# Optimization experiments

Measured on AMD Instinct MI355X. Metric: run time of the kernel, lower is better.

The kernel has to match this reference:

```python
import jax, jax.numpy as jnp
import numpy as np

N_NODES = 100000
N_EDGES = 1600000
D_IN = 256
D_HID = 128
N_CLASSES = 64
NEG_SLOPE = 0.2


def setup_inputs() -> dict:
    key = jax.random.key(0)
    ks = jax.random.split(key, 8)
    node_features = jax.random.normal(ks[0], (N_NODES, D_IN), dtype=jnp.float32)
    W = jax.random.normal(ks[1], (D_IN, D_HID), dtype=jnp.float32) * (1.0 / np.sqrt(D_IN))
    attn_l = jax.random.normal(ks[2], (D_HID,), dtype=jnp.float32) * (1.0 / np.sqrt(D_HID))
    attn_r = jax.random.normal(ks[3], (D_HID,), dtype=jnp.float32) * (1.0 / np.sqrt(D_HID))
    fc_W = jax.random.normal(ks[4], (D_HID, N_CLASSES), dtype=jnp.float32) * (1.0 / np.sqrt(D_HID))
    fc_b = jnp.zeros((N_CLASSES,), dtype=jnp.float32)
    src = jax.random.randint(ks[5], (N_EDGES,), 0, N_NODES, dtype=jnp.int32)
    dst = jax.random.randint(ks[6], (N_EDGES,), 0, N_NODES, dtype=jnp.int32)
    return dict(node_features=node_features, W=W, attn_l=attn_l, attn_r=attn_r,
                fc_W=fc_W, fc_b=fc_b, src=src, dst=dst)


def reference(node_features, W, attn_l, attn_r, fc_W, fc_b, src, dst):
    N = node_features.shape[0]
    # GATConv (single head): linear projection
    feat = node_features @ W                       # [N, H]
    el = feat @ attn_l                             # [N]
    er = feat @ attn_r                             # [N]
    e = jax.nn.leaky_relu(el[src] + er[dst], NEG_SLOPE)  # [E]
    # segment softmax over incoming edges of each destination node
    m = jax.ops.segment_max(e, dst, num_segments=N)      # [N]
    ex = jnp.exp(e - m[dst])                              # [E]
    denom = jax.ops.segment_sum(ex, dst, num_segments=N)  # [N]
    a = ex / denom[dst]                                   # [E]
    # attention-weighted neighbor aggregation (scatter-add)
    msg = a[:, None] * feat[src]                           # [E, H]
    h = jax.ops.segment_sum(msg, dst, num_segments=N)     # [N, H]
    # num_heads=1 -> h.mean(1) over heads is identity; final Linear
    return h @ fc_W + fc_b                                 # [N, C]
```

## Files before the change

### kernel.cpp

```cpp
#include <hip/hip_runtime.h>
#include <math.h>

#define NN 100000
#define NE 1600000
#define DIN 256
#define DHID 128
#define NCLS 64
#define NEG_SLOPE 0.2f

#define NBUCK 196
#define ECAP 10240
#define CHUNK 4096
#define NCHB ((NE + CHUNK - 1) / CHUNK)
#define PREPB 16

#define NGRP 16384
#define G1 ((NN + 127) / 128)

typedef __bf16 bf16_t;
typedef bf16_t bf16x8 __attribute__((ext_vector_type(8)));
typedef float f32x4 __attribute__((ext_vector_type(4)));
typedef ushort ushort8v __attribute__((ext_vector_type(8)));

__device__ __forceinline__ ushort f2bf(float f) {
    union { float f; unsigned u; } c; c.f = f;
    unsigned u = c.u;
    unsigned r = (u + 0x7FFFu + ((u >> 16) & 1u)) >> 16;
    return (ushort)r;
}
__device__ __forceinline__ float bf2f(ushort b) {
    return __uint_as_float(((unsigned)b) << 16);
}

__global__ __launch_bounds__(256) void k_prep(const float* __restrict__ W,
                                              const float* __restrict__ fcW,
                                              ushort* __restrict__ Wt,
                                              ushort* __restrict__ fcWt,
                                              int* __restrict__ gcur) {
    int t = blockIdx.x * 256 + threadIdx.x;
    if (blockIdx.x == 0) gcur[threadIdx.x] = 0;
    for (int i = t; i < DHID * DIN; i += PREPB * 256) {
        int n = i >> 8, k = i & 255;
        Wt[i] = f2bf(W[k * DHID + n]);
    }
    for (int i = t; i < NCLS * DHID; i += PREPB * 256) {
        int n = i >> 7, k = i & 127;
        fcWt[i] = f2bf(fcW[k * NCLS + n]);
    }
}

union SmemB {
    struct {
        int hist[NBUCK];
        int scn[256];
        int loff[NBUCK];
        int cur[NBUCK];
        int gb[NBUCK];
        unsigned ord[CHUNK];
        ushort obk[CHUNK];
    } b;
    struct {
        ushort Xs[2][8192];
        ushort Wl[2][8192];
        float Al[DHID];
        float Ar[DHID];
    } g;
};

__global__ __launch_bounds__(256, 2) void fused_bin_gemm1(
        const int* __restrict__ src, const int* __restrict__ dst,
        int* __restrict__ gcur, unsigned* __restrict__ ebuf,
        const float* __restrict__ X, const ushort* __restrict__ Wt,
        const float* __restrict__ attn_l, const float* __restrict__ attn_r,
        ushort* __restrict__ featb, float* __restrict__ el, float* __restrict__ er) {
    __shared__ SmemB sm;
    const int t = threadIdx.x;

    if (blockIdx.x < NCHB) {
        const int base = blockIdx.x * CHUNK;
        int cnt = NE - base; if (cnt > CHUNK) cnt = CHUNK;

        for (int i = t; i < NBUCK; i += 256) sm.b.hist[i] = 0;
        __syncthreads();

        unsigned vals[16];
        int bks[16];
#pragma unroll
        for (int i = 0; i < 16; i++) {
            int idx = base + i * 256 + t;
            if (idx < NE) {
                int d = dst[idx], s = src[idx];
                int bb = d >> 9;
                bks[i] = bb;
                vals[i] = ((unsigned)(d & 511) << 17) | (unsigned)s;
                atomicAdd(&sm.b.hist[bb], 1);
            } else bks[i] = -1;
        }
        __syncthreads();

        int hv = (t < NBUCK) ? sm.b.hist[t] : 0;
        sm.b.scn[t] = hv;
        __syncthreads();
        for (int d = 1; d < 256; d <<= 1) {
            int a = (t >= d) ? sm.b.scn[t - d] : 0;
            __syncthreads();
            sm.b.scn[t] += a;
            __syncthreads();
        }
        if (t < NBUCK) { sm.b.loff[t] = sm.b.scn[t] - hv; sm.b.cur[t] = sm.b.scn[t] - hv; }
        __syncthreads();

#pragma unroll
        for (int i = 0; i < 16; i++) {
            if (bks[i] >= 0) {
                int slot = atomicAdd(&sm.b.cur[bks[i]], 1);
                sm.b.ord[slot] = vals[i];
                sm.b.obk[slot] = (ushort)bks[i];
            }
        }
        if (t < NBUCK && hv > 0) sm.b.gb[t] = t * ECAP + atomicAdd(&gcur[t], hv);
        __syncthreads();

        for (int s = t; s < cnt; s += 256) {
            int bb = sm.b.obk[s];
            ebuf[sm.b.gb[bb] + (s - sm.b.loff[bb])] = sm.b.ord[s];
        }
        return;
    }

    const int row0 = (blockIdx.x - NCHB) * 128;
    if (t < 128) { sm.g.Al[t] = attn_l[t]; sm.g.Ar[t] = attn_r[t]; }

    int srow[4], ske[4];
#pragma unroll
    for (int i = 0; i < 4; i++) {
        int o = i * 4096 + t * 16;
        int row = o >> 7;
        int bl = (o & 127) ^ ((row & 7) << 4);
        srow[i] = row;
        ske[i] = bl >> 1;
    }

    float4 xr[4][2];
    uint4  wr[4];

#pragma unroll
    for (int i = 0; i < 4; i++) {
        int grow = row0 + srow[i];
        if (grow < NN) {
            const float4* p = (const float4*)(X + (size_t)grow * DIN + ske[i]);
            xr[i][0] = p[0]; xr[i][1] = p[1];
        } else {
            xr[i][0] = make_float4(0.f, 0.f, 0.f, 0.f);
            xr[i][1] = make_float4(0.f, 0.f, 0.f, 0.f);
        }
        wr[i] = *(const uint4*)(Wt + (size_t)srow[i] * DIN + ske[i]);
    }
#pragma unroll
    for (int i = 0; i < 4; i++) {
        int o = i * 4096 + t * 16;
        ushort8v b;
        b[0] = f2bf(xr[i][0].x); b[1] = f2bf(xr[i][0].y);
        b[2] = f2bf(xr[i][0].z); b[3] = f2bf(xr[i][0].w);
        b[4] = f2bf(xr[i][1].x); b[5] = f2bf(xr[i][1].y);
        b[6] = f2bf(xr[i][1].z); b[7] = f2bf(xr[i][1].w);
        *(ushort8v*)((char*)&sm.g.Xs[0][0] + o) = b;
        *(uint4*)((char*)&sm.g.Wl[0][0] + o) = wr[i];
    }
    __syncthreads();

    const int w = t >> 6, lane = t & 63;
    const int rbase = w * 32;
    const int lcol = lane & 15;
    const int kgrp = (lane >> 4) * 16;

    f32x4 acc[2][8];
#pragma unroll
    for (int r = 0; r < 2; r++)
#pragma unroll
        for (int c = 0; c < 8; c++) acc[r][c] = (f32x4){0.f, 0.f, 0.f, 0.f};

    for (int c = 0; c < 4; c++) {
        const int buf = c & 1;
        if (c < 3) {
            int k0g = (c + 1) * 64;
#pragma unroll
            for (int i = 0; i < 4; i++) {
                int grow = row0 + srow[i];
                if (grow < NN) {
                    const float4* p = (const float4*)(X + (size_t)grow * DIN + k0g + ske[i]);
                    xr[i][0] = p[0]; xr[i][1] = p[1];
                } else {
                    xr[i][0] = make_float4(0.f, 0.f, 0.f, 0.f);
                    xr[i][1] = make_float4(0.f, 0.f, 0.f, 0.f);
                }
                wr[i] = *(const uint4*)(Wt + (size_t)srow[i] * DIN + k0g + ske[i]);
            }
        }
        const char* xb = (const char*)&sm.g.Xs[buf][0];
        const char* wb = (const char*)&sm.g.Wl[buf][0];
#pragma unroll
        for (int k0 = 0; k0 < 2; k0++) {
            int kb = k0 * 64 + kgrp;
            bf16x8 a[2], b[8];
#pragma unroll
            for (int r = 0; r < 2; r++) {
                int row = rbase + r * 16 + lcol;
                a[r] = *(const bf16x8*)(xb + row * 128 + (kb ^ ((row & 7) << 4)));
            }
#pragma unroll
            for (int cc = 0; cc < 8; cc++) {
                int n = cc * 16 + lcol;
                b[cc] = *(const bf16x8*)(wb + n * 128 + (kb ^ ((n & 7) << 4)));
            }
#pragma unroll
            for (int r = 0; r < 2; r++)
#pragma unroll
                for (int cc = 0; cc < 8; cc++)
                    acc[r][cc] = __builtin_amdgcn_mfma_f32_16x16x32_bf16(a[r], b[cc], acc[r][cc], 0, 0, 0);
        }
        if (c < 3) {
#pragma unroll
            for (int i = 0; i < 4; i++) {
                int o = i * 4096 + t * 16;
                ushort8v b;
                b[0] = f2bf(xr[i][0].x); b[1] = f2bf(xr[i][0].y);
                b[2] = f2bf(xr[i][0].z); b[3] = f2bf(xr[i][0].w);
                b[4] = f2bf(xr[i][1].x); b[5] = f2bf(xr[i][1].y);
                b[6] = f2bf(xr[i][1].z); b[7] = f2bf(xr[i][1].w);
                *(ushort8v*)((char*)&sm.g.Xs[buf ^ 1][0] + o) = b;
                *(uint4*)((char*)&sm.g.Wl[buf ^ 1][0] + o) = wr[i];
            }
        }
        __syncthreads();
    }

    ushort* Os = (ushort*)sm.g.Xs;
#pragma unroll
    for (int r = 0; r < 2; r++)
#pragma unroll
        for (int cc = 0; cc < 8; cc++)
#pragma unroll
            for (int i = 0; i < 4; i++) {
                int rloc = rbase + r * 16 + (lane >> 4) * 4 + i;
                int col = cc * 16 + lcol;
                Os[rloc * 128 + col] = f2bf(acc[r][cc][i]);
            }
    __syncthreads();

    {
        int row = t >> 1, half = t & 1;
        int grow = row0 + row;
        const ushort* orow = Os + row * 128 + half * 64;
        const float* alp = sm.g.Al + half * 64;
        const float* arp = sm.g.Ar + half * 64;
        float pl = 0.f, pr = 0.f;
        int rot = row & 7;
#pragma unroll
        for (int qq = 0; qq < 8; qq++) {
            int q = (qq + rot) & 7;
            ushort8v f8 = *(const ushort8v*)(orow + q * 8);
#pragma unroll
            for (int e = 0; e < 8; e++) {
                float fe = bf2f(f8[e]);
                pl += fe * alp[q * 8 + e];
                pr += fe * arp[q * 8 + e];
            }
        }
        pl += __shfl_down(pl, 1);
        pr += __shfl_down(pr, 1);
        if (!half && grow < NN) { el[grow] = pl; er[grow] = pr; }
    }

#pragma unroll
    for (int i = 0; i < 8; i++) {
        int u = i * 256 + t;
        int row = u >> 4;
        int grow = row0 + row;
        if (grow < NN)
            *(uint4*)(featb + (size_t)grow * 128 + (u & 15) * 8) =
                *(uint4*)((char*)Os + u * 16);
    }
}

union SmemC {
    struct {
        int sdeg[512];
        int pr[256];
        int lofs[512];
        int scnt[512];
    } c;
    int sh[256];
};

__global__ __launch_bounds__(256) void fused_csr(const unsigned* __restrict__ ebuf,
                                                 const int* __restrict__ gcur,
                                                 int* __restrict__ off_g,
                                                 int* __restrict__ deg_g,
                                                 int* __restrict__ ssrc,
                                                 int* __restrict__ bpre) {
    __shared__ SmemC sm;
    const int t = threadIdx.x;

    if (blockIdx.x == NBUCK) {
        int v = (t < NBUCK) ? gcur[t] : 0;
        sm.sh[t] = v;
        __syncthreads();
        for (int d = 1; d < 256; d <<= 1) {
            int a = (t >= d) ? sm.sh[t - d] : 0;
            __syncthreads();
            sm.sh[t] += a;
            __syncthreads();
        }
        if (t < NBUCK) bpre[t] = sm.sh[t] - v;
        if (t == NBUCK - 1) bpre[NBUCK] = sm.sh[t];
        return;
    }

    const int b = blockIdx.x;
    const int node0 = b << 9;
    const int ebase = b * ECAP;
    const int ecnt = gcur[b];

    sm.c.sdeg[t] = 0; sm.c.sdeg[t + 256] = 0;
    __syncthreads();
    for (int s = t; s < ecnt; s += 256)
        atomicAdd(&sm.c.sdeg[ebuf[ebase + s] >> 17], 1);
    __syncthreads();

    int d0 = sm.c.sdeg[2 * t], d1 = sm.c.sdeg[2 * t + 1];
    sm.c.pr[t] = d0 + d1;
    __syncthreads();
    for (int d = 1; d < 256; d <<= 1) {
        int a = (t >= d) ? sm.c.pr[t - d] : 0;
        __syncthreads();
        sm.c.pr[t] += a;
        __syncthreads();
    }
    int ex = sm.c.pr[t] - d0 - d1;
    sm.c.lofs[2 * t] = ex;
    sm.c.lofs[2 * t + 1] = ex + d0;
    sm.c.scnt[2 * t] = 0; sm.c.scnt[2 * t + 1] = 0;
    int n0 = node0 + 2 * t, n1 = n0 + 1;
    if (n0 < NN) { off_g[n0] = ebase + ex;      deg_g[n0] = d0; }
    if (n1 < NN) { off_g[n1] = ebase + ex + d0; deg_g[n1] = d1; }
    __syncthreads();

    for (int s = t; s < ecnt; s += 256) {
        unsigned v = ebuf[ebase + s];
        int dl = v >> 17;
        int c = atomicAdd(&sm.c.scnt[dl], 1);
        ssrc[ebase + sm.c.lofs[dl] + c] = (int)(v & 0x1FFFFu);
    }
}

__device__ __forceinline__ int find_node(const int* __restrict__ off,
                                         const int* __restrict__ bpre,
                                         long target) {
    int lo = 0, hi = NN;
    while (lo < hi) {
        int mid = (lo + hi) >> 1;
        int b = mid >> 9;
        long real = (long)off[mid] - (long)b * ECAP + bpre[b];
        if (real < target) lo = mid + 1; else hi = mid;
    }
    return lo;
}

__global__ __launch_bounds__(256) void aggregate(const int* __restrict__ off,
                                                 const int* __restrict__ deg,
                                                 const int* __restrict__ ssrc,
                                                 const float* __restrict__ el,
                                                 const float* __restrict__ er,
                                                 const ushort* __restrict__ featb,
                                                 ushort* __restrict__ hb,
                                                 const int* __restrict__ bpre) {
    const int gid = blockIdx.x * 16 + (threadIdx.x >> 4);
    const int lc = threadIdx.x & 15;
    const long total = bpre[NBUCK];
    int n = find_node(off, bpre, (long)gid * total / NGRP);
    const int nend = find_node(off, bpre, (long)(gid + 1) * total / NGRP);
    const ushort* fb = featb + lc * 8;

    for (; n < nend; ++n) {
        const int e0 = off[n];
        const int dg = deg[n];
        const float erd = er[n];
        float acc[8];
#pragma unroll
        for (int q = 0; q < 8; q++) acc[q] = 0.f;
        float wsum = 0.f;

        int j = 0;
        for (; j + 4 <= dg; j += 4) {
            int s0 = ssrc[e0 + j + 0];
            int s1 = ssrc[e0 + j + 1];
            int s2 = ssrc[e0 + j + 2];
            int s3 = ssrc[e0 + j + 3];
            ushort8v f0 = *(const ushort8v*)(fb + (size_t)s0 * DHID);
            ushort8v f1 = *(const ushort8v*)(fb + (size_t)s1 * DHID);
            ushort8v f2 = *(const ushort8v*)(fb + (size_t)s2 * DHID);
            ushort8v f3 = *(const ushort8v*)(fb + (size_t)s3 * DHID);
            float x0 = el[s0] + erd, x1 = el[s1] + erd;
            float x2 = el[s2] + erd, x3 = el[s3] + erd;
            x0 = x0 > 0.f ? x0 : NEG_SLOPE * x0;
            x1 = x1 > 0.f ? x1 : NEG_SLOPE * x1;
            x2 = x2 > 0.f ? x2 : NEG_SLOPE * x2;
            x3 = x3 > 0.f ? x3 : NEG_SLOPE * x3;
            float w0 = __expf(x0), w1 = __expf(x1);
            float w2 = __expf(x2), w3 = __expf(x3);
            wsum += (w0 + w1) + (w2 + w3);
#pragma unroll
            for (int q = 0; q < 8; q++)
                acc[q] += (w0 * bf2f(f0[q]) + w1 * bf2f(f1[q])) +
                          (w2 * bf2f(f2[q]) + w3 * bf2f(f3[q]));
        }
        for (; j < dg; ++j) {
            int s0 = ssrc[e0 + j];
            ushort8v f0 = *(const ushort8v*)(fb + (size_t)s0 * DHID);
            float x0 = el[s0] + erd;
            x0 = x0 > 0.f ? x0 : NEG_SLOPE * x0;
            float w0 = __expf(x0);
            wsum += w0;
#pragma unroll
            for (int q = 0; q < 8; q++) acc[q] += w0 * bf2f(f0[q]);
        }

        float inv = (dg > 0) ? 1.0f / wsum : 0.f;
        ushort8v o8;
#pragma unroll
        for (int q = 0; q < 8; q++) o8[q] = f2bf(acc[q] * inv);
        *(ushort8v*)(hb + (size_t)n * DHID + lc * 8) = o8;
    }
}

__global__ __launch_bounds__(256) void gemm2(const ushort* __restrict__ hb,
                                             const ushort* __restrict__ fcWt,
                                             const float* __restrict__ fcb,
                                             float* __restrict__ out) {
    __shared__ ushort Hs[128 * 128];
    __shared__ ushort Fs[64 * 128];
    const int t = threadIdx.x;
    const int row0 = blockIdx.x * 128;

    {
#pragma unroll
        for (int i = 0; i < 8; i++) {
            int u = i * 256 + t;
            int row = u >> 4;
            int grow = row0 + row;
            uint4 v = make_uint4(0, 0, 0, 0);
            if (grow < NN) v = *(const uint4*)(hb + (size_t)grow * 128 + (u & 15) * 8);
            int byte_off = row * 256 + (((u & 15) * 16) ^ ((row & 7) << 4));
            *(uint4*)((char*)Hs + byte_off) = v;
        }
#pragma unroll
        for (int i = 0; i < 4; i++) {
            int u = i * 256 + t;
            int n = u >> 4;
            int byte_off = n * 256 + (((u & 15) * 16) ^ ((n & 7) << 4));
            *(uint4*)((char*)Fs + byte_off) = ((const uint4*)fcWt)[u];
        }
    }

    const int w = t >> 6, lane = t & 63;
    const int rbase = w * 32;
    const int lcol = lane & 15;
    const int kgrp = (lane >> 4) * 16;

    f32x4 acc[2][4];
#pragma unroll
    for (int c = 0; c < 4; c++) {
        float bias = fcb[c * 16 + lcol];
#pragma unroll
        for (int r = 0; r < 2; r++)
#pragma unroll
            for (int i = 0; i < 4; i++) acc[r][c][i] = bias;
    }
    __syncthreads();

#pragma unroll
    for (int k0 = 0; k0 < 4; k0++) {
        int kbyte = k0 * 64 + kgrp;
        bf16x8 a[2], b[4];
#pragma unroll
        for (int r = 0; r < 2; r++) {
            int row = rbase + r * 16 + lcol;
            a[r] = *(bf16x8*)((char*)Hs + row * 256 + (kbyte ^ ((row & 7) << 4)));
        }
#pragma unroll
        for (int c = 0; c < 4; c++) {
            int n = c * 16 + lcol;
            b[c] = *(bf16x8*)((char*)Fs + n * 256 + (kbyte ^ ((n & 7) << 4)));
        }
#pragma unroll
        for (int r = 0; r < 2; r++)
#pragma unroll
            for (int c = 0; c < 4; c++)
                acc[r][c] = __builtin_amdgcn_mfma_f32_16x16x32_bf16(a[r], b[c], acc[r][c], 0, 0, 0);
    }

#pragma unroll
    for (int r = 0; r < 2; r++)
#pragma unroll
        for (int i = 0; i < 4; i++) {
            int row = rbase + r * 16 + (lane >> 4) * 4 + i;
            int grow = row0 + row;
            if (grow < NN) {
                float* op = out + (size_t)grow * 64 + lcol;
#pragma unroll
                for (int c = 0; c < 4; c++) op[c * 16] = acc[r][c][i];
            }
        }
}

extern "C" void kernel_launch(void* const* d_in, const int* in_sizes, int n_in,
                              void* d_out, int out_size, void* d_ws, size_t ws_size,
                              hipStream_t stream) {
    const float* X      = (const float*)d_in[0];
    const float* W      = (const float*)d_in[1];
    const float* attn_l = (const float*)d_in[2];
    const float* attn_r = (const float*)d_in[3];
    const float* fcW    = (const float*)d_in[4];
    const float* fcb    = (const float*)d_in[5];
    const int*   src    = (const int*)d_in[6];
    const int*   dst    = (const int*)d_in[7];
    float* out = (float*)d_out;

    char* ws = (char*)d_ws;
    ushort* featb = (ushort*)ws;            ws += (size_t)NN * DHID * 2;
    ushort* hb    = (ushort*)ws;            ws += (size_t)NN * DHID * 2;
    ushort* Wt    = (ushort*)ws;            ws += (size_t)DHID * DIN * 2;
    ushort* fcWt  = (ushort*)ws;            ws += (size_t)NCLS * DHID * 2;
    float* el     = (float*)ws;             ws += (size_t)NN * 4;
    float* er     = (float*)ws;             ws += (size_t)NN * 4;
    int*   deg    = (int*)ws;               ws += (size_t)NN * 4;
    int*   off    = (int*)ws;               ws += (size_t)NN * 4;
    int*   ssrc   = (int*)ws;               ws += (size_t)NBUCK * ECAP * 4;
    unsigned* ebuf = (unsigned*)ws;         ws += (size_t)NBUCK * ECAP * 4;
    int*   gcur   = (int*)ws;               ws += (size_t)256 * 4;
    int*   bpre   = (int*)ws;               ws += (size_t)256 * 4;

    k_prep<<<PREPB, 256, 0, stream>>>(W, fcW, Wt, fcWt, gcur);
    fused_bin_gemm1<<<NCHB + G1, 256, 0, stream>>>(src, dst, gcur, ebuf,
                                                   X, Wt, attn_l, attn_r, featb, el, er);
    fused_csr<<<NBUCK + 1, 256, 0, stream>>>(ebuf, gcur, off, deg, ssrc, bpre);
    aggregate<<<NGRP / 16, 256, 0, stream>>>(off, deg, ssrc, el, er, featb, hb, bpre);
    gemm2<<<(NN + 127) / 128, 256, 0, stream>>>(hb, fcWt, fcb, out);
}
```

Measured before the change: 160.4 us.

## Regroup kernels: fuse binning with weight prep, GEMM1 with CSR build

The weight transpose/convert kernel is folded into the edge-binning kernel as extra blocks, and the CSR construction moves into the GEMM1 launch. GEMM1 now loads X and W fragments straight from global memory into registers with a software pipeline, dropping the LDS staging buffers and per-stage barriers. gcur is zeroed with a memset, and gemm2 gets an occupancy hint in its launch bounds. The aim is fewer launches and better overlap of independent work, at the cost of uncoalesced direct-to-register loads and more register pressure in GEMM1.

Measured after the change: 170.4 us. +6.2%, slower.

```diff
diff --git a/kernel.cpp b/kernel.cpp
--- a/kernel.cpp
+++ b/kernel.cpp
@@ -31,25 +31,14 @@
 __device__ __forceinline__ float bf2f(ushort b) {
     return __uint_as_float(((unsigned)b) << 16);
 }
-
-__global__ __launch_bounds__(256) void k_prep(const float* __restrict__ W,
-                                              const float* __restrict__ fcW,
-                                              ushort* __restrict__ Wt,
-                                              ushort* __restrict__ fcWt,
-                                              int* __restrict__ gcur) {
-    int t = blockIdx.x * 256 + threadIdx.x;
-    if (blockIdx.x == 0) gcur[threadIdx.x] = 0;
-    for (int i = t; i < DHID * DIN; i += PREPB * 256) {
-        int n = i >> 8, k = i & 255;
-        Wt[i] = f2bf(W[k * DHID + n]);
-    }
-    for (int i = t; i < NCLS * DHID; i += PREPB * 256) {
-        int n = i >> 7, k = i & 127;
-        fcWt[i] = f2bf(fcW[k * NCLS + n]);
-    }
-}
-
-union SmemB {
+__device__ __forceinline__ bf16x8 cvt8(float4 a, float4 b) {
+    union { ushort8v u; bf16x8 h; } c;
+    c.u[0] = f2bf(a.x); c.u[1] = f2bf(a.y); c.u[2] = f2bf(a.z); c.u[3] = f2bf(a.w);
+    c.u[4] = f2bf(b.x); c.u[5] = f2bf(b.y); c.u[6] = f2bf(b.z); c.u[7] = f2bf(b.w);
+    return c.h;
+}
+
+union SmemA {
     struct {
         int hist[NBUCK];
         int scn[256];
@@ -59,191 +48,221 @@
         unsigned ord[CHUNK];
         ushort obk[CHUNK];
     } b;
+};
+
+__global__ __launch_bounds__(256) void fused_bin_prep(
+        const int* __restrict__ src, const int* __restrict__ dst,
+        int* __restrict__ gcur, unsigned* __restrict__ ebuf,
+        const float* __restrict__ W, const float* __restrict__ fcW,
+        ushort* __restrict__ Wt, ushort* __restrict__ fcWt) {
+    __shared__ SmemA sm;
+    const int t = threadIdx.x;
+
+    if (blockIdx.x >= NCHB) {
+        int t0 = (blockIdx.x - NCHB) * 256 + t;
+        for (int i = t0; i < DHID * DIN; i += PREPB * 256) {
+            int n = i >> 8, k = i & 255;
+            Wt[i] = f2bf(W[k * DHID + n]);
+        }
+        for (int i = t0; i < NCLS * DHID; i += PREPB * 256) {
+            int n = i >> 7, k = i & 127;
+            fcWt[i] = f2bf(fcW[k * NCLS + n]);
+        }
+        return;
+    }
+
+    const int base = blockIdx.x * CHUNK;
+    int cnt = NE - base; if (cnt > CHUNK) cnt = CHUNK;
+
+    for (int i = t; i < NBUCK; i += 256) sm.b.hist[i] = 0;
+    __syncthreads();
+
+    unsigned vals[16];
+    int bks[16];
+#pragma unroll
+    for (int i = 0; i < 16; i++) {
+        int idx = base + i * 256 + t;
+        if (idx < NE) {
+            int d = dst[idx], s = src[idx];
+            int bb = d >> 9;
+            bks[i] = bb;
+            vals[i] = ((unsigned)(d & 511) << 17) | (unsigned)s;
+            atomicAdd(&sm.b.hist[bb], 1);
+        } else bks[i] = -1;
+    }
+    __syncthreads();
+
+    int hv = (t < NBUCK) ? sm.b.hist[t] : 0;
+    sm.b.scn[t] = hv;
+    __syncthreads();
+    for (int d = 1; d < 256; d <<= 1) {
+        int a = (t >= d) ? sm.b.scn[t - d] : 0;
+        __syncthreads();
+        sm.b.scn[t] += a;
+        __syncthreads();
+    }
+    if (t < NBUCK) { sm.b.loff[t] = sm.b.scn[t] - hv; sm.b.cur[t] = sm.b.scn[t] - hv; }
+    __syncthreads();
+
+#pragma unroll
+    for (int i = 0; i < 16; i++) {
+        if (bks[i] >= 0) {
+            int slot = atomicAdd(&sm.b.cur[bks[i]], 1);
+            sm.b.ord[slot] = vals[i];
+            sm.b.obk[slot] = (ushort)bks[i];
+        }
+    }
+    if (t < NBUCK && hv > 0) sm.b.gb[t] = t * ECAP + atomicAdd(&gcur[t], hv);
+    __syncthreads();
+
+    for (int s = t; s < cnt; s += 256) {
+        int bb = sm.b.obk[s];
+        ebuf[sm.b.gb[bb] + (s - sm.b.loff[bb])] = sm.b.ord[s];
+    }
+}
+
+union SmemB {
     struct {
-        ushort Xs[2][8192];
-        ushort Wl[2][8192];
+        ushort Os[128 * 128];
         float Al[DHID];
         float Ar[DHID];
     } g;
+    struct {
+        int sdeg[512];
+        int pr[256];
+        int lofs[512];
+        int scnt[512];
+    } c;
+    int sh[256];
 };
 
-__global__ __launch_bounds__(256, 2) void fused_bin_gemm1(
-        const int* __restrict__ src, const int* __restrict__ dst,
-        int* __restrict__ gcur, unsigned* __restrict__ ebuf,
+#define LOADX(B, KS) do { \
+    if (v0) { xa[B][0][0] = *(const float4*)(xb0 + (KS) * 32); \
+              xa[B][0][1] = *(const float4*)(xb0 + (KS) * 32 + 4); } \
+    else { xa[B][0][0] = make_float4(0.f,0.f,0.f,0.f); xa[B][0][1] = make_float4(0.f,0.f,0.f,0.f); } \
+    if (v1) { xa[B][1][0] = *(const float4*)(xb1 + (KS) * 32); \
+              xa[B][1][1] = *(const float4*)(xb1 + (KS) * 32 + 4); } \
+    else { xa[B][1][0] = make_float4(0.f,0.f,0.f,0.f); xa[B][1][1] = make_float4(0.f,0.f,0.f,0.f); } \
+} while (0)
+
+#define LOADW(B, KS) do { \
+    _Pragma("unroll") \
+    for (int cc = 0; cc < 8; cc++) \
+        bw[B][cc] = *(const bf16x8*)(wb + cc * 4096 + (KS) * 32); \
+} while (0)
+
+#define GITER(KS) do { \
+    if ((KS) + 1 < 8) LOADW(((KS) + 1) & 1, (KS) + 1); \
+    { bf16x8 af0 = cvt8(xa[(KS) % 3][0][0], xa[(KS) % 3][0][1]); \
+      bf16x8 af1 = cvt8(xa[(KS) % 3][1][0], xa[(KS) % 3][1][1]); \
+      _Pragma("unroll") \
+      for (int cc = 0; cc < 8; cc++) { \
+          acc[0][cc] = __builtin_amdgcn_mfma_f32_16x16x32_bf16(af0, bw[(KS) & 1][cc], acc[0][cc], 0, 0, 0); \
+          acc[1][cc] = __builtin_amdgcn_mfma_f32_16x16x32_bf16(af1, bw[(KS) & 1][cc], acc[1][cc], 0, 0, 0); } } \
+    if ((KS) + 3 < 8) LOADX((KS) % 3, (KS) + 3); \
+} while (0)
+
+__global__ __launch_bounds__(256, 2) void fused_g1_csr(
         const float* __restrict__ X, const ushort* __restrict__ Wt,
         const float* __restrict__ attn_l, const float* __restrict__ attn_r,
-        ushort* __restrict__ featb, float* __restrict__ el, float* __restrict__ er) {
+        ushort* __restrict__ featb, float* __restrict__ el, float* __restrict__ er,
+        const unsigned* __restrict__ ebuf, const int* __restrict__ gcur,
+        int* __restrict__ off_g, int* __restrict__ deg_g,
+        int* __restrict__ ssrc, int* __restrict__ bpre) {
     __shared__ SmemB sm;
     const int t = threadIdx.x;
 
-    if (blockIdx.x < NCHB) {
-        const int base = blockIdx.x * CHUNK;
-        int cnt = NE - base; if (cnt > CHUNK) cnt = CHUNK;
-
-        for (int i = t; i < NBUCK; i += 256) sm.b.hist[i] = 0;
-        __syncthreads();
-
-        unsigned vals[16];
-        int bks[16];
-#pragma unroll
-        for (int i = 0; i < 16; i++) {
-            int idx = base + i * 256 + t;
-            if (idx < NE) {
-                int d = dst[idx], s = src[idx];
-                int bb = d >> 9;
-                bks[i] = bb;
-                vals[i] = ((unsigned)(d & 511) << 17) | (unsigned)s;
-                atomicAdd(&sm.b.hist[bb], 1);
-            } else bks[i] = -1;
-        }
-        __syncthreads();
-
-        int hv = (t < NBUCK) ? sm.b.hist[t] : 0;
-        sm.b.scn[t] = hv;
+    if (blockIdx.x >= G1 + NBUCK) {
+        int v = (t < NBUCK) ? gcur[t] : 0;
+        sm.sh[t] = v;
         __syncthreads();
         for (int d = 1; d < 256; d <<= 1) {
-            int a = (t >= d) ? sm.b.scn[t - d] : 0;
+            int a = (t >= d) ? sm.sh[t - d] : 0;
             __syncthreads();
-            sm.b.scn[t] += a;
+            sm.sh[t] += a;
             __syncthreads();
         }
-        if (t < NBUCK) { sm.b.loff[t] = sm.b.scn[t] - hv; sm.b.cur[t] = sm.b.scn[t] - hv; }
-        __syncthreads();
-
-#pragma unroll
-        for (int i = 0; i < 16; i++) {
-            if (bks[i] >= 0) {
-                int slot = atomicAdd(&sm.b.cur[bks[i]], 1);
-                sm.b.ord[slot] = vals[i];
-                sm.b.obk[slot] = (ushort)bks[i];
-            }
-        }
-        if (t < NBUCK && hv > 0) sm.b.gb[t] = t * ECAP + atomicAdd(&gcur[t], hv);
-        __syncthreads();
-
-        for (int s = t; s < cnt; s += 256) {
-            int bb = sm.b.obk[s];
-            ebuf[sm.b.gb[bb] + (s - sm.b.loff[bb])] = sm.b.ord[s];
-        }
+        if (t < NBUCK) bpre[t] = sm.sh[t] - v;
+        if (t == NBUCK - 1) bpre[NBUCK] = sm.sh[t];
         return;
     }
 
-    const int row0 = (blockIdx.x - NCHB) * 128;
+    if (blockIdx.x >= G1) {
+        const int b = blockIdx.x - G1;
+        const int node0 = b << 9;
+        const int ebase = b * ECAP;
+        const int ecnt = gcur[b];
+
+        sm.c.sdeg[t] = 0; sm.c.sdeg[t + 256] = 0;
+        __syncthreads();
+        for (int s = t; s < ecnt; s += 256)
+            atomicAdd(&sm.c.sdeg[ebuf[ebase + s] >> 17], 1);
+        __syncthreads();
+
+        int d0 = sm.c.sdeg[2 * t], d1 = sm.c.sdeg[2 * t + 1];
+        sm.c.pr[t] = d0 + d1;
+        __syncthreads();
+        for (int d = 1; d < 256; d <<= 1) {
+            int a = (t >= d) ? sm.c.pr[t - d] : 0;
+            __syncthreads();
+            sm.c.pr[t] += a;
+            __syncthreads();
+        }
+        int ex = sm.c.pr[t] - d0 - d1;
+        sm.c.lofs[2 * t] = ex;
+        sm.c.lofs[2 * t + 1] = ex + d0;
+        sm.c.scnt[2 * t] = 0; sm.c.scnt[2 * t + 1] = 0;
+        int n0 = node0 + 2 * t, n1 = n0 + 1;
+        if (n0 < NN) { off_g[n0] = ebase + ex;      deg_g[n0] = d0; }
+        if (n1 < NN) { off_g[n1] = ebase + ex + d0; deg_g[n1] = d1; }
+        __syncthreads();
+
+        for (int s = t; s < ecnt; s += 256) {
+            unsigned v = ebuf[ebase + s];
+            int dl = v >> 17;
+            int c = atomicAdd(&sm.c.scnt[dl], 1);
+            ssrc[ebase + sm.c.lofs[dl] + c] = (int)(v & 0x1FFFFu);
+        }
+        return;
+    }
+
+    const int row0 = blockIdx.x * 128;
     if (t < 128) { sm.g.Al[t] = attn_l[t]; sm.g.Ar[t] = attn_r[t]; }
-
-    int srow[4], ske[4];
-#pragma unroll
-    for (int i = 0; i < 4; i++) {
-        int o = i * 4096 + t * 16;
-        int row = o >> 7;
-        int bl = (o & 127) ^ ((row & 7) << 4);
-        srow[i] = row;
-        ske[i] = bl >> 1;
-    }
-
-    float4 xr[4][2];
-    uint4  wr[4];
-
-#pragma unroll
-    for (int i = 0; i < 4; i++) {
-        int grow = row0 + srow[i];
-        if (grow < NN) {
-            const float4* p = (const float4*)(X + (size_t)grow * DIN + ske[i]);
-            xr[i][0] = p[0]; xr[i][1] = p[1];
-        } else {
-            xr[i][0] = make_float4(0.f, 0.f, 0.f, 0.f);
-            xr[i][1] = make_float4(0.f, 0.f, 0.f, 0.f);
-        }
-        wr[i] = *(const uint4*)(Wt + (size_t)srow[i] * DIN + ske[i]);
-    }
-#pragma unroll
-    for (int i = 0; i < 4; i++) {
-        int o = i * 4096 + t * 16;
-        ushort8v b;
-        b[0] = f2bf(xr[i][0].x); b[1] = f2bf(xr[i][0].y);
-        b[2] = f2bf(xr[i][0].z); b[3] = f2bf(xr[i][0].w);
-        b[4] = f2bf(xr[i][1].x); b[5] = f2bf(xr[i][1].y);
-        b[6] = f2bf(xr[i][1].z); b[7] = f2bf(xr[i][1].w);
-        *(ushort8v*)((char*)&sm.g.Xs[0][0] + o) = b;
-        *(uint4*)((char*)&sm.g.Wl[0][0] + o) = wr[i];
-    }
-    __syncthreads();
 
     const int w = t >> 6, lane = t & 63;
     const int rbase = w * 32;
-    const int lcol = lane & 15;
-    const int kgrp = (lane >> 4) * 16;
-
+    const int lc16 = lane & 15;
+    const int kg = lane >> 4;
+
+    const int arow0 = row0 + rbase + lc16;
+    const int arow1 = arow0 + 16;
+    const bool v0 = arow0 < NN, v1 = arow1 < NN;
+    const float* xb0 = X + (size_t)arow0 * DIN + kg * 8;
+    const float* xb1 = X + (size_t)arow1 * DIN + kg * 8;
+    const ushort* wb = Wt + (size_t)lc16 * DIN + kg * 8;
+
+    float4 xa[3][2][2];
+    bf16x8 bw[2][8];
     f32x4 acc[2][8];
 #pragma unroll
     for (int r = 0; r < 2; r++)
 #pragma unroll
         for (int c = 0; c < 8; c++) acc[r][c] = (f32x4){0.f, 0.f, 0.f, 0.f};
 
-    for (int c = 0; c < 4; c++) {
-        const int buf = c & 1;
-        if (c < 3) {
-            int k0g = (c + 1) * 64;
+    LOADX(0, 0); LOADX(1, 1); LOADX(2, 2);
+    LOADW(0, 0);
+    GITER(0); GITER(1); GITER(2); GITER(3);
+    GITER(4); GITER(5); GITER(6); GITER(7);
+
+    ushort* Os = sm.g.Os;
+#pragma unroll
+    for (int r = 0; r < 2; r++)
+#pragma unroll
+        for (int cc = 0; cc < 8; cc++)
 #pragma unroll
             for (int i = 0; i < 4; i++) {
-                int grow = row0 + srow[i];
-                if (grow < NN) {
-                    const float4* p = (const float4*)(X + (size_t)grow * DIN + k0g + ske[i]);
-                    xr[i][0] = p[0]; xr[i][1] = p[1];
-                } else {
-                    xr[i][0] = make_float4(0.f, 0.f, 0.f, 0.f);
-                    xr[i][1] = make_float4(0.f, 0.f, 0.f, 0.f);
-                }
-                wr[i] = *(const uint4*)(Wt + (size_t)srow[i] * DIN + k0g + ske[i]);
-            }
-        }
-        const char* xb = (const char*)&sm.g.Xs[buf][0];
-        const char* wb = (const char*)&sm.g.Wl[buf][0];
-#pragma unroll
-        for (int k0 = 0; k0 < 2; k0++) {
-            int kb = k0 * 64 + kgrp;
-            bf16x8 a[2], b[8];
-#pragma unroll
-            for (int r = 0; r < 2; r++) {
-                int row = rbase + r * 16 + lcol;
-                a[r] = *(const bf16x8*)(xb + row * 128 + (kb ^ ((row & 7) << 4)));
-            }
-#pragma unroll
-            for (int cc = 0; cc < 8; cc++) {
-                int n = cc * 16 + lcol;
-                b[cc] = *(const bf16x8*)(wb + n * 128 + (kb ^ ((n & 7) << 4)));
-            }
-#pragma unroll
-            for (int r = 0; r < 2; r++)
-#pragma unroll
-                for (int cc = 0; cc < 8; cc++)
-                    acc[r][cc] = __builtin_amdgcn_mfma_f32_16x16x32_bf16(a[r], b[cc], acc[r][cc], 0, 0, 0);
-        }
-        if (c < 3) {
-#pragma unroll
-            for (int i = 0; i < 4; i++) {
-                int o = i * 4096 + t * 16;
-                ushort8v b;
-                b[0] = f2bf(xr[i][0].x); b[1] = f2bf(xr[i][0].y);
-                b[2] = f2bf(xr[i][0].z); b[3] = f2bf(xr[i][0].w);
-                b[4] = f2bf(xr[i][1].x); b[5] = f2bf(xr[i][1].y);
-                b[6] = f2bf(xr[i][1].z); b[7] = f2bf(xr[i][1].w);
-                *(ushort8v*)((char*)&sm.g.Xs[buf ^ 1][0] + o) = b;
-                *(uint4*)((char*)&sm.g.Wl[buf ^ 1][0] + o) = wr[i];
-            }
-        }
-        __syncthreads();
-    }
-
-    ushort* Os = (ushort*)sm.g.Xs;
-#pragma unroll
-    for (int r = 0; r < 2; r++)
-#pragma unroll
-        for (int cc = 0; cc < 8; cc++)
-#pragma unroll
-            for (int i = 0; i < 4; i++) {
-                int rloc = rbase + r * 16 + (lane >> 4) * 4 + i;
-                int col = cc * 16 + lcol;
+                int rloc = rbase + r * 16 + kg * 4 + i;
+                int col = cc * 16 + lc16;
                 Os[rloc * 128 + col] = f2bf(acc[r][cc][i]);
             }
     __syncthreads();
@@ -280,77 +299,6 @@
         if (grow < NN)
             *(uint4*)(featb + (size_t)grow * 128 + (u & 15) * 8) =
                 *(uint4*)((char*)Os + u * 16);
-    }
-}
-
-union SmemC {
-    struct {
-        int sdeg[512];
-        int pr[256];
-        int lofs[512];
-        int scnt[512];
-    } c;
-    int sh[256];
-};
-
-__global__ __launch_bounds__(256) void fused_csr(const unsigned* __restrict__ ebuf,
-                                                 const int* __restrict__ gcur,
-                                                 int* __restrict__ off_g,
-                                                 int* __restrict__ deg_g,
-                                                 int* __restrict__ ssrc,
-                                                 int* __restrict__ bpre) {
-    __shared__ SmemC sm;
-    const int t = threadIdx.x;
-
-    if (blockIdx.x == NBUCK) {
-        int v = (t < NBUCK) ? gcur[t] : 0;
-        sm.sh[t] = v;
-        __syncthreads();
-        for (int d = 1; d < 256; d <<= 1) {
-            int a = (t >= d) ? sm.sh[t - d] : 0;
-            __syncthreads();
-            sm.sh[t] += a;
-            __syncthreads();
-        }
-        if (t < NBUCK) bpre[t] = sm.sh[t] - v;
-        if (t == NBUCK - 1) bpre[NBUCK] = sm.sh[t];
-        return;
-    }
-
-    const int b = blockIdx.x;
-    const int node0 = b << 9;
-    const int ebase = b * ECAP;
-    const int ecnt = gcur[b];
-
-    sm.c.sdeg[t] = 0; sm.c.sdeg[t + 256] = 0;
-    __syncthreads();
-    for (int s = t; s < ecnt; s += 256)
-        atomicAdd(&sm.c.sdeg[ebuf[ebase + s] >> 17], 1);
-    __syncthreads();
-
-    int d0 = sm.c.sdeg[2 * t], d1 = sm.c.sdeg[2 * t + 1];
-    sm.c.pr[t] = d0 + d1;
-    __syncthreads();
-    for (int d = 1; d < 256; d <<= 1) {
-        int a = (t >= d) ? sm.c.pr[t - d] : 0;
-        __syncthreads();
-        sm.c.pr[t] += a;
-        __syncthreads();
-    }
-    int ex = sm.c.pr[t] - d0 - d1;
-    sm.c.lofs[2 * t] = ex;
-    sm.c.lofs[2 * t + 1] = ex + d0;
-    sm.c.scnt[2 * t] = 0; sm.c.scnt[2 * t + 1] = 0;
-    int n0 = node0 + 2 * t, n1 = n0 + 1;
-    if (n0 < NN) { off_g[n0] = ebase + ex;      deg_g[n0] = d0; }
-    if (n1 < NN) { off_g[n1] = ebase + ex + d0; deg_g[n1] = d1; }
-    __syncthreads();
-
-    for (int s = t; s < ecnt; s += 256) {
-        unsigned v = ebuf[ebase + s];
-        int dl = v >> 17;
-        int c = atomicAdd(&sm.c.scnt[dl], 1);
-        ssrc[ebase + sm.c.lofs[dl] + c] = (int)(v & 0x1FFFFu);
     }
 }
 
@@ -434,10 +382,10 @@
     }
 }
 
-__global__ __launch_bounds__(256) void gemm2(const ushort* __restrict__ hb,
-                                             const ushort* __restrict__ fcWt,
-                                             const float* __restrict__ fcb,
-                                             float* __restrict__ out) {
+__global__ __launch_bounds__(256, 3) void gemm2(const ushort* __restrict__ hb,
+                                                const ushort* __restrict__ fcWt,
+                                                const float* __restrict__ fcb,
+                                                float* __restrict__ out) {
     __shared__ ushort Hs[128 * 128];
     __shared__ ushort Fs[64 * 128];
     const int t = threadIdx.x;
@@ -541,10 +489,11 @@
     int*   gcur   = (int*)ws;               ws += (size_t)256 * 4;
     int*   bpre   = (int*)ws;               ws += (size_t)256 * 4;
 
-    k_prep<<<PREPB, 256, 0, stream>>>(W, fcW, Wt, fcWt, gcur);
-    fused_bin_gemm1<<<NCHB + G1, 256, 0, stream>>>(src, dst, gcur, ebuf,
-                                                   X, Wt, attn_l, attn_r, featb, el, er);
-    fused_csr<<<NBUCK + 1, 256, 0, stream>>>(ebuf, gcur, off, deg, ssrc, bpre);
+    hipMemsetAsync(gcur, 0, NBUCK * sizeof(int), stream);
+
+    fused_bin_prep<<<NCHB + PREPB, 256, 0, stream>>>(src, dst, gcur, ebuf, W, fcW, Wt, fcWt);
+    fused_g1_csr<<<G1 + NBUCK + 1, 256, 0, stream>>>(X, Wt, attn_l, attn_r, featb, el, er,
+                                                     ebuf, gcur, off, deg, ssrc, bpre);
     aggregate<<<NGRP / 16, 256, 0, stream>>>(off, deg, ssrc, el, er, featb, hb, bpre);
     gemm2<<<(NN + 127) / 128, 256, 0, stream>>>(hb, fcWt, fcb, out);
 }
```
